# Kernel optimization log

Hardware: AMD Instinct MI355X
Metric: run time of the kernel (lower is better)

The kernel has to match this reference:

```python
import jax, jax.numpy as jnp
import numpy as np

LN_EPS = 1e-5


def layer_norm(x, gamma, beta):
    mu = jnp.mean(x, axis=-1, keepdims=True)
    var = jnp.mean(jnp.square(x - mu), axis=-1, keepdims=True)
    return (x - mu) * jax.lax.rsqrt(var + LN_EPS) * gamma + beta


def setup_inputs() -> dict:
    key = jax.random.key(0)
    ks = jax.random.split(key, 4)
    b, t, d, h, r = 4, 2048, 1024, 4096, 32
    x = jax.random.normal(ks[0], (b, t, d), dtype=jnp.float32)
    L = jax.random.normal(ks[1], (d, r), dtype=jnp.float32) * (1.0 / np.sqrt(d))
    W1 = jax.random.normal(ks[2], (d, h), dtype=jnp.float32) * (1.0 / np.sqrt(d))
    W2 = jax.random.normal(ks[3], (h, d), dtype=jnp.float32) * (1.0 / np.sqrt(h))
    return {
        "x": x, "L": L,
        "W1": W1, "b1": jnp.zeros((h,), jnp.float32),
        "W2": W2, "b2": jnp.zeros((d,), jnp.float32),
        "gamma1": jnp.ones((d,), jnp.float32), "beta1": jnp.zeros((d,), jnp.float32),
        "gamma2": jnp.ones((d,), jnp.float32), "beta2": jnp.zeros((d,), jnp.float32),
    }


def reference(x, L, W1, b1, W2, b2, gamma1, beta1, gamma2, beta2):
    d = x.shape[-1]
    # --- GeodesicAttention on norm1(x) ---
    hn = layer_norm(x, gamma1, beta1)  # (b,t,d)
    g = jnp.eye(d, dtype=x.dtype) + L @ L.T  # PSD metric G = I + L L^T, (d,d)
    # dist_sq[b,i,j] = (x_i - x_j)^T G (x_i - x_j)
    #               = q_i + q_j - 2 x_i^T G x_j   (quadratic expansion; avoids (b,t,t,d) diff tensor)
    xg = jnp.einsum('btd,de->bte', hn, g)          # G x, (b,t,d)
    q = jnp.einsum('btd,btd->bt', xg, hn)          # diag quadratic form, (b,t)
    cross = jnp.einsum('bid,bjd->bij', xg, hn)     # x_i^T G x_j, (b,t,t)
    dist_sq = q[:, :, None] + q[:, None, :] - 2.0 * cross
    attn = jax.nn.softmax(-dist_sq, axis=-1)       # (b,t,t)
    x = x + jnp.einsum('bij,bjd->bid', attn, hn)
    # --- MLP on norm2(x) ---
    hm = layer_norm(x, gamma2, beta2)
    hid = jax.nn.gelu(hm @ W1 + b1, approximate=False)
    x = x + hid @ W2 + b2
    return x
```

## Files before the change

kernel.cpp:

```cpp
#include <hip/hip_runtime.h>
#include <cstdint>

typedef float f32x4 __attribute__((ext_vector_type(4)));
typedef __bf16 bf16x8 __attribute__((ext_vector_type(8)));

#define AS1 __attribute__((address_space(1)))
#define AS3 __attribute__((address_space(3)))

__device__ __forceinline__ void gld_lds16(const void* g, void* l) {
    __builtin_amdgcn_global_load_lds((const AS1 void*)g, (AS3 void*)l, 16, 0, 0);
}

__device__ __forceinline__ unsigned short f2bf(float f) {
    unsigned u = __builtin_bit_cast(unsigned, f);
    u = u + 0x7fffu + ((u >> 16) & 1u);
    return (unsigned short)(u >> 16);
}
__device__ __forceinline__ float bf2f(unsigned short h) {
    unsigned u = ((unsigned)h) << 16;
    return __builtin_bit_cast(float, u);
}

__device__ __forceinline__ void bar() {
    asm volatile("" ::: "memory");
    __builtin_amdgcn_s_barrier();
    asm volatile("" ::: "memory");
}

#define WAITVM(n) asm volatile("s_waitcnt vmcnt(" #n ")" ::: "memory")
#define LGKM0     asm volatile("s_waitcnt lgkmcnt(0)" ::: "memory")
#define SCHED0    __builtin_amdgcn_sched_barrier(0)

template<int BN, int MODE>
__global__ __launch_bounds__(512, 2) void gemm8p(
    const unsigned short* __restrict__ A, long lda, long sAb,
    const unsigned short* __restrict__ B, long ldb, long sBb,
    void* C, long ldc, long sCb,
    const float* add, long ldadd, long sAddb,
    const float* __restrict__ bias, int K)
{
    constexpr int NR   = BN / 64;
    constexpr int ABUF = 256 * 128;
    constexpr int BBUF = BN * 128;
    constexpr int BUF  = ABUF + BBUF;
    __shared__ char sm[2 * BUF];
    const int tid = threadIdx.x, lane = tid & 63, wid = tid >> 6;
    const int wr = wid >> 2, wc = wid & 3;

    const long zb = blockIdx.z;
    const int nwg  = gridDim.x * gridDim.y;
    const int orig = blockIdx.y * gridDim.x + blockIdx.x;
    const int q8 = nwg >> 3, r8 = nwg & 7;
    const int xcd = orig & 7;
    const int wg  = (xcd < r8 ? xcd * (q8 + 1) : r8 * (q8 + 1) + (xcd - r8) * q8) + (orig >> 3);
    const int bx = wg % gridDim.x, by = wg / gridDim.x;

    const char* Ab = (const char*)(A + zb * sAb + (long)by * 256 * lda);
    const char* Bb = (const char*)(B + zb * sBb + (long)bx * BN * ldb);
    const long ldaB = lda * 2, ldbB = ldb * 2;

    auto stageA = [&](int kt, int p, int half) {
#pragma unroll
        for (int i = 0; i < 2; ++i) {
            const int r0 = half * 64 + i * 128;
            const int r  = r0 + (tid >> 3);
            gld_lds16(Ab + (long)r * ldaB + (long)kt * 128 + (((tid & 7) ^ (r & 7)) << 4),
                      sm + p * BUF + r0 * 128 + wid * 1024);
        }
    };
    auto stageB = [&](int kt, int p, int ks) {
#pragma unroll
        for (int i = 0; i < BN / 128; ++i) {
            const int r = i * 128 + (tid >> 2);
            gld_lds16(Bb + (long)r * ldbB + (long)kt * 128 + ks * 64 + (((tid & 3) ^ ((r >> 1) & 3)) << 4),
                      sm + p * BUF + ABUF + ks * BN * 64 + i * 8192 + wid * 1024);
        }
    };

    f32x4 acc[8][NR] = {};
    const int NT = K / 64;

#define PHASE(MH, KS, STAGE_STMT) do {                                          \
    bf16x8 af[4]; bf16x8 bfr[NR];                                               \
    _Pragma("unroll")                                                           \
    for (int m = 0; m < 4; ++m) {                                               \
        const int R = wr * 128 + ((MH) * 4 + m) * 16 + (lane & 15);             \
        const int cc = (((KS) * 4 + (lane >> 4)) ^ (R & 7)) << 4;               \
        af[m] = *(const bf16x8*)(bufp + R * 128 + cc);                          \
    }                                                                           \
    _Pragma("unroll")                                                           \
    for (int n = 0; n < NR; ++n) {                                              \
        const int R = wc * 16 * NR + n * 16 + (lane & 15);                      \
        const int cc = ((lane >> 4) ^ ((R >> 1) & 3)) << 4;                     \
        bfr[n] = *(const bf16x8*)(bufp + ABUF + (KS) * BN * 64 + R * 64 + cc);  \
    }                                                                           \
    STAGE_STMT;                                                                 \
    if (t < NT - 2) { if constexpr (BN == 256) WAITVM(8); else WAITVM(6); }     \
    else WAITVM(0);                                                             \
    bar();                                                                      \
    LGKM0; SCHED0;                                                              \
    __builtin_amdgcn_s_setprio(1);                                              \
    _Pragma("unroll")                                                           \
    for (int m = 0; m < 4; ++m)                                                 \
    _Pragma("unroll")                                                           \
        for (int n = 0; n < NR; ++n)                                            \
            acc[(MH) * 4 + m][n] = __builtin_amdgcn_mfma_f32_16x16x32_bf16(     \
                af[m], bfr[n], acc[(MH) * 4 + m][n], 0, 0, 0);                  \
    __builtin_amdgcn_s_setprio(0);                                              \
    bar();                                                                      \
} while (0)

    stageA(0, 0, 0); stageA(0, 0, 1); stageB(0, 0, 0); stageB(0, 0, 1);
    stageA(1, 1, 0); stageB(1, 1, 0); stageA(1, 1, 1); stageB(1, 1, 1);
    if constexpr (BN == 256) WAITVM(8); else WAITVM(6);
    bar();

#pragma unroll 1
    for (int t = 0; t < NT; ++t) {
        const int p = t & 1;
        const char* bufp = sm + p * BUF;
        PHASE(0, 0, { if (t >= 1 && t + 1 < NT) stageA(t + 1, p ^ 1, 1); });
        PHASE(1, 0, { if (t >= 1 && t + 1 < NT) stageB(t + 1, p ^ 1, 1); });
        PHASE(0, 1, { if (t + 2 < NT) stageB(t + 2, p, 0); });
        PHASE(1, 1, { if (t + 2 < NT) stageA(t + 2, p, 0); });
    }
#undef PHASE

    const long row0 = (long)by * 256 + wr * 128 + (lane >> 4) * 4;
    const long col0 = (long)bx * BN + wc * 16 * NR + (lane & 15);
#pragma unroll
    for (int m = 0; m < 8; ++m)
#pragma unroll
        for (int n = 0; n < NR; ++n)
#pragma unroll
            for (int j = 0; j < 4; ++j) {
                const long r = row0 + m * 16 + j;
                const long c = col0 + n * 16;
                const float v = acc[m][n][j];
                if (MODE == 0) {
                    ((float*)C)[zb * sCb + r * ldc + c] = v;
                } else if (MODE == 1) {
                    ((float*)C)[zb * sCb + r * ldc + c] = v + add[zb * sAddb + r * ldadd + c];
                } else if (MODE == 2) {
                    float tt = v + bias[c];
                    float gl = 0.5f * tt * (1.0f + erff(tt * 0.70710678118654752f));
                    ((unsigned short*)C)[zb * sCb + r * ldc + c] = f2bf(gl);
                } else {
                    ((float*)C)[zb * sCb + r * ldc + c] = v + bias[c] + add[zb * sAddb + r * ldadd + c];
                }
            }
}

__global__ __launch_bounds__(256) void ln_kernel(
    const float* __restrict__ x, const float* __restrict__ gamma, const float* __restrict__ beta,
    unsigned short* __restrict__ out, int ldout, float* qout, int pad)
{
    const int tid = threadIdx.x;
    const long row = blockIdx.x;
    float4 v = ((const float4*)(x + row * 1024))[tid];
    float s = v.x + v.y + v.z + v.w;
    float s2 = v.x * v.x + v.y * v.y + v.z * v.z + v.w * v.w;
#pragma unroll
    for (int off = 32; off; off >>= 1) {
        s  += __shfl_down(s, off);
        s2 += __shfl_down(s2, off);
    }
    __shared__ float red[12];
    const int lane = tid & 63, wid = tid >> 6;
    if (lane == 0) { red[wid] = s; red[4 + wid] = s2; }
    __syncthreads();
    s  = red[0] + red[1] + red[2] + red[3];
    s2 = red[4] + red[5] + red[6] + red[7];
    const float mu = s * (1.0f / 1024.0f);
    const float var = s2 * (1.0f / 1024.0f) - mu * mu;
    const float rs = rsqrtf(var + 1e-5f);
    const float4 g = ((const float4*)gamma)[tid];
    const float4 b = ((const float4*)beta)[tid];
    unsigned short o0 = f2bf((v.x - mu) * rs * g.x + b.x);
    unsigned short o1 = f2bf((v.y - mu) * rs * g.y + b.y);
    unsigned short o2 = f2bf((v.z - mu) * rs * g.z + b.z);
    unsigned short o3 = f2bf((v.w - mu) * rs * g.w + b.w);
    ushort4 ov; ov.x = o0; ov.y = o1; ov.z = o2; ov.w = o3;
    ((ushort4*)(out + row * (long)ldout))[tid] = ov;
    if (pad && tid < 32) out[row * (long)ldout + 1056 + tid] = 0;
    if (qout) {
        float y0 = bf2f(o0), y1 = bf2f(o1), y2 = bf2f(o2), y3 = bf2f(o3);
        float sq = y0 * y0 + y1 * y1 + y2 * y2 + y3 * y3;
#pragma unroll
        for (int off = 32; off; off >>= 1) sq += __shfl_down(sq, off);
        if (lane == 0) red[8 + wid] = sq;
        __syncthreads();
        if (tid == 0) qout[row] = red[8] + red[9] + red[10] + red[11];
    }
}

__global__ __launch_bounds__(256) void u_kernel(
    unsigned short* __restrict__ z, const float* __restrict__ L, float* __restrict__ q)
{
    const int tid = threadIdx.x;
    const long row = blockIdx.x;
    __shared__ float hn[1024];
    __shared__ float part[8][32];
    ushort4 uv = ((const ushort4*)(z + row * 1088))[tid];
    hn[tid * 4 + 0] = bf2f(uv.x);
    hn[tid * 4 + 1] = bf2f(uv.y);
    hn[tid * 4 + 2] = bf2f(uv.z);
    hn[tid * 4 + 3] = bf2f(uv.w);
    __syncthreads();
    const int j = tid & 31, grp = tid >> 5;
    float acc = 0.f;
    const float* Lp = L + j;
#pragma unroll 4
    for (int d = grp * 128; d < grp * 128 + 128; ++d)
        acc += hn[d] * Lp[(long)d * 32];
    part[grp][j] = acc;
    __syncthreads();
    if (tid < 32) {
        float u = 0.f;
#pragma unroll
        for (int g2 = 0; g2 < 8; ++g2) u += part[g2][tid];
        unsigned short ub = f2bf(u);
        z[row * 1088 + 1024 + tid] = ub;
        float uf = bf2f(ub);
        part[0][tid] = uf * uf;
    }
    __syncthreads();
    if (tid == 0) {
        float sq = 0.f;
#pragma unroll
        for (int t2 = 0; t2 < 32; ++t2) sq += part[0][t2];
        q[row] += sq;
    }
}

__global__ __launch_bounds__(256) void softmax_kernel(
    float* S, const float* qb)
{
    const int tid = threadIdx.x;
    const long i = blockIdx.x, bl = blockIdx.y;
    float* Sr = S + (bl * 2048 + i) * 2048;
    const float* qr = qb + bl * 2048;
    float l[8];
    float mx = -1e30f;
#pragma unroll
    for (int c2 = 0; c2 < 8; ++c2) {
        const int jj = tid + c2 * 256;
        l[c2] = 2.0f * Sr[jj] - qr[jj];
        mx = fmaxf(mx, l[c2]);
    }
#pragma unroll
    for (int off = 32; off; off >>= 1) mx = fmaxf(mx, __shfl_xor(mx, off));
    __shared__ float red[8];
    const int lane = tid & 63, wid = tid >> 6;
    if (lane == 0) red[wid] = mx;
    __syncthreads();
    mx = fmaxf(fmaxf(red[0], red[1]), fmaxf(red[2], red[3]));
    float sum = 0.f;
#pragma unroll
    for (int c2 = 0; c2 < 8; ++c2) { l[c2] = __expf(l[c2] - mx); sum += l[c2]; }
#pragma unroll
    for (int off = 32; off; off >>= 1) sum += __shfl_xor(sum, off);
    if (lane == 0) red[4 + wid] = sum;
    __syncthreads();
    sum = red[4] + red[5] + red[6] + red[7];
    const float inv = 1.0f / sum;
    unsigned short* Pr = (unsigned short*)S + (bl * 2048 + i) * 4096;
#pragma unroll
    for (int c2 = 0; c2 < 8; ++c2)
        Pr[tid + c2 * 256] = f2bf(l[c2] * inv);
}

__global__ __launch_bounds__(256) void transpose_v_kernel(
    const unsigned short* __restrict__ z, unsigned short* __restrict__ Vt, long sVtb)
{
    __shared__ unsigned short t[32][33];
    const int tid = threadIdx.x;
    const int tx = tid & 31, ty = tid >> 5;
    const long b = blockIdx.z;
    const long k0 = (long)blockIdx.x * 32, n0 = (long)blockIdx.y * 32;
#pragma unroll
    for (int r = 0; r < 32; r += 8)
        t[r + ty][tx] = z[(b * 2048 + k0 + r + ty) * 1088 + n0 + tx];
    __syncthreads();
#pragma unroll
    for (int r = 0; r < 32; r += 8)
        Vt[b * sVtb + (n0 + r + ty) * 2048 + k0 + tx] = t[tx][r + ty];
}

__global__ __launch_bounds__(256) void cast_transpose_kernel(
    const float* __restrict__ W, unsigned short* __restrict__ Wt, int rows, int cols)
{
    __shared__ float t[32][33];
    const int tid = threadIdx.x;
    const int tx = tid & 31, ty = tid >> 5;
    const long r0 = (long)blockIdx.y * 32, c0 = (long)blockIdx.x * 32;
#pragma unroll
    for (int r = 0; r < 32; r += 8)
        t[r + ty][tx] = W[(r0 + r + ty) * (long)cols + c0 + tx];
    __syncthreads();
#pragma unroll
    for (int r = 0; r < 32; r += 8)
        Wt[(c0 + r + ty) * (long)rows + r0 + tx] = f2bf(t[tx][r + ty]);
}

extern "C" void kernel_launch(void* const* d_in, const int* in_sizes, int n_in,
                              void* d_out, int out_size, void* d_ws, size_t ws_size,
                              hipStream_t stream)
{
    const float* x   = (const float*)d_in[0];
    const float* L   = (const float*)d_in[1];
    const float* W1  = (const float*)d_in[2];
    const float* b1  = (const float*)d_in[3];
    const float* W2  = (const float*)d_in[4];
    const float* b2  = (const float*)d_in[5];
    const float* g1  = (const float*)d_in[6];
    const float* be1 = (const float*)d_in[7];
    const float* g2  = (const float*)d_in[8];
    const float* be2 = (const float*)d_in[9];
    float* out = (float*)d_out;
    unsigned short* z = (unsigned short*)d_out;

    char* wsp = (char*)d_ws;
    float* q = (float*)wsp;
    char* pool = wsp + 32768;
    unsigned short* Vt   = (unsigned short*)pool;
    float*          Smat = (float*)(pool + 16777216);
    unsigned short* W1t = (unsigned short*)pool;
    unsigned short* W2t = (unsigned short*)(pool + 8388608);
    unsigned short* hm  = (unsigned short*)(pool + 16777216);
    unsigned short* hid = (unsigned short*)(pool + 33554432);
    const bool fullMLP = ws_size >= (size_t)32768 + 100663296 + 65536;

    ln_kernel<<<8192, 256, 0, stream>>>(x, g1, be1, z, 1088, q, 1);
    u_kernel<<<8192, 256, 0, stream>>>(z, L, q);

    transpose_v_kernel<<<dim3(64, 32, 4), 256, 0, stream>>>(z, Vt, (long)1024 * 2048);
    gemm8p<256, 0><<<dim3(8, 8, 4), 512, 0, stream>>>(
        z, 1088, (long)2048 * 1088,
        z, 1088, (long)2048 * 1088,
        Smat, 2048, (long)2048 * 2048,
        nullptr, 0, 0, nullptr, 1088);
    softmax_kernel<<<dim3(2048, 4), 256, 0, stream>>>(Smat, q);
    gemm8p<128, 1><<<dim3(8, 8, 4), 512, 0, stream>>>(
        (const unsigned short*)Smat, 4096, (long)2048 * 4096,
        Vt, 2048, (long)1024 * 2048,
        out, 1024, (long)2048 * 1024,
        x, 1024, (long)2048 * 1024,
        nullptr, 2048);

    cast_transpose_kernel<<<dim3(128, 32), 256, 0, stream>>>(W1, W1t, 1024, 4096);
    cast_transpose_kernel<<<dim3(32, 128), 256, 0, stream>>>(W2, W2t, 4096, 1024);
    ln_kernel<<<8192, 256, 0, stream>>>(out, g2, be2, hm, 1024, nullptr, 0);
    if (fullMLP) {
        gemm8p<256, 2><<<dim3(16, 32, 1), 512, 0, stream>>>(
            hm, 1024, 0, W1t, 1024, 0,
            hid, 4096, 0, nullptr, 0, 0, b1, 1024);
        gemm8p<128, 3><<<dim3(8, 32, 1), 512, 0, stream>>>(
            hid, 4096, 0, W2t, 4096, 0,
            out, 1024, 0, out, 1024, 0, b2, 4096);
    } else {
        for (int c = 0; c < 2; ++c) {
            const unsigned short* hmc = hm + (size_t)c * 4096 * 1024;
            float* oc = out + (size_t)c * 4096 * 1024;
            gemm8p<256, 2><<<dim3(16, 16, 1), 512, 0, stream>>>(
                hmc, 1024, 0, W1t, 1024, 0,
                hid, 4096, 0, nullptr, 0, 0, b1, 1024);
            gemm8p<128, 3><<<dim3(8, 16, 1), 512, 0, stream>>>(
                hid, 4096, 0, W2t, 4096, 0,
                oc, 1024, 0, oc, 1024, 0, b2, 4096);
        }
    }
}
```

Before: 389.5 us.

## Restructure GEMM prefetch waits and add XCD-aware tile swizzle for attention GEMMs

Changes the GEMM software pipeline so the prologue only preloads half of tile 1 and the loop issues the remaining stages every iteration. The vmcnt wait moves from every phase to one wait per K-tile at the last phase, which cuts per-phase stalls. Separately, a new swizzle mode maps the batched 8x8x4 attention GEMM grid so that each XCD gets a 2x4 block of neighbouring tiles within one batch, improving L2 reuse. The risk is that the wait counts are tightly coupled to the load ordering, and a miscount would cause stale LDS reads.

```diff
diff --git a/kernel.cpp b/kernel.cpp
--- a/kernel.cpp
+++ b/kernel.cpp
@@ -31,8 +31,8 @@
 #define LGKM0     asm volatile("s_waitcnt lgkmcnt(0)" ::: "memory")
 #define SCHED0    __builtin_amdgcn_sched_barrier(0)
 
-template<int BN, int MODE>
-__global__ __launch_bounds__(512, 2) void gemm8p(
+template<int BN, int MODE, int SWZ>
+__global__ __launch_bounds__(512, 2) void gemm8q(
     const unsigned short* __restrict__ A, long lda, long sAb,
     const unsigned short* __restrict__ B, long ldb, long sBb,
     void* C, long ldc, long sCb,
@@ -47,13 +47,24 @@
     const int tid = threadIdx.x, lane = tid & 63, wid = tid >> 6;
     const int wr = wid >> 2, wc = wid & 3;
 
-    const long zb = blockIdx.z;
-    const int nwg  = gridDim.x * gridDim.y;
-    const int orig = blockIdx.y * gridDim.x + blockIdx.x;
-    const int q8 = nwg >> 3, r8 = nwg & 7;
-    const int xcd = orig & 7;
-    const int wg  = (xcd < r8 ? xcd * (q8 + 1) : r8 * (q8 + 1) + (xcd - r8) * q8) + (orig >> 3);
-    const int bx = wg % gridDim.x, by = wg / gridDim.x;
+    int bx, by;
+    long zb;
+    if constexpr (SWZ == 1) {
+        const int d   = blockIdx.x + ((blockIdx.y + (blockIdx.z << 3)) << 3);
+        const int xcd = d & 7, j = d >> 3;
+        zb = j >> 3;
+        const int pos = j & 7;
+        by = ((xcd & 1) << 2) + (pos >> 1);
+        bx = ((xcd >> 1) << 1) + (pos & 1);
+    } else {
+        zb = blockIdx.z;
+        const int nwg  = gridDim.x * gridDim.y;
+        const int orig = blockIdx.y * gridDim.x + blockIdx.x;
+        const int q8 = nwg >> 3, r8 = nwg & 7;
+        const int xcd = orig & 7;
+        const int wg  = (xcd < r8 ? xcd * (q8 + 1) : r8 * (q8 + 1) + (xcd - r8) * q8) + (orig >> 3);
+        bx = wg % gridDim.x; by = wg / gridDim.x;
+    }
 
     const char* Ab = (const char*)(A + zb * sAb + (long)by * 256 * lda);
     const char* Bb = (const char*)(B + zb * sBb + (long)bx * BN * ldb);
@@ -80,7 +91,7 @@
     f32x4 acc[8][NR] = {};
     const int NT = K / 64;
 
-#define PHASE(MH, KS, STAGE_STMT) do {                                          \
+#define PHASE(MH, KS, STAGE_STMT, WAIT_STMT) do {                               \
     bf16x8 af[4]; bf16x8 bfr[NR];                                               \
     _Pragma("unroll")                                                           \
     for (int m = 0; m < 4; ++m) {                                               \
@@ -95,8 +106,7 @@
         bfr[n] = *(const bf16x8*)(bufp + ABUF + (KS) * BN * 64 + R * 64 + cc);  \
     }                                                                           \
     STAGE_STMT;                                                                 \
-    if (t < NT - 2) { if constexpr (BN == 256) WAITVM(8); else WAITVM(6); }     \
-    else WAITVM(0);                                                             \
+    WAIT_STMT;                                                                  \
     bar();                                                                      \
     LGKM0; SCHED0;                                                              \
     __builtin_amdgcn_s_setprio(1);                                              \
@@ -111,18 +121,20 @@
 } while (0)
 
     stageA(0, 0, 0); stageA(0, 0, 1); stageB(0, 0, 0); stageB(0, 0, 1);
-    stageA(1, 1, 0); stageB(1, 1, 0); stageA(1, 1, 1); stageB(1, 1, 1);
-    if constexpr (BN == 256) WAITVM(8); else WAITVM(6);
+    if (NT > 1) { stageB(1, 1, 0); stageA(1, 1, 0); }
+    if constexpr (BN == 256) WAITVM(4); else WAITVM(3);
     bar();
 
 #pragma unroll 1
     for (int t = 0; t < NT; ++t) {
         const int p = t & 1;
         const char* bufp = sm + p * BUF;
-        PHASE(0, 0, { if (t >= 1 && t + 1 < NT) stageA(t + 1, p ^ 1, 1); });
-        PHASE(1, 0, { if (t >= 1 && t + 1 < NT) stageB(t + 1, p ^ 1, 1); });
-        PHASE(0, 1, { if (t + 2 < NT) stageB(t + 2, p, 0); });
-        PHASE(1, 1, { if (t + 2 < NT) stageA(t + 2, p, 0); });
+        PHASE(0, 0, { if (t + 1 < NT) stageA(t + 1, p ^ 1, 1); }, {});
+        PHASE(1, 0, { if (t + 1 < NT) stageB(t + 1, p ^ 1, 1); }, {});
+        PHASE(0, 1, { if (t + 2 < NT) stageB(t + 2, p, 0); }, {});
+        PHASE(1, 1, { if (t + 2 < NT) stageA(t + 2, p, 0); },
+              { if (t + 2 < NT) { if constexpr (BN == 256) WAITVM(4); else WAITVM(3); }
+                else if (t + 1 < NT) WAITVM(0); });
     }
 #undef PHASE
 
@@ -335,13 +347,13 @@
     u_kernel<<<8192, 256, 0, stream>>>(z, L, q);
 
     transpose_v_kernel<<<dim3(64, 32, 4), 256, 0, stream>>>(z, Vt, (long)1024 * 2048);
-    gemm8p<256, 0><<<dim3(8, 8, 4), 512, 0, stream>>>(
+    gemm8q<256, 0, 1><<<dim3(8, 8, 4), 512, 0, stream>>>(
         z, 1088, (long)2048 * 1088,
         z, 1088, (long)2048 * 1088,
         Smat, 2048, (long)2048 * 2048,
         nullptr, 0, 0, nullptr, 1088);
     softmax_kernel<<<dim3(2048, 4), 256, 0, stream>>>(Smat, q);
-    gemm8p<128, 1><<<dim3(8, 8, 4), 512, 0, stream>>>(
+    gemm8q<128, 1, 1><<<dim3(8, 8, 4), 512, 0, stream>>>(
         (const unsigned short*)Smat, 4096, (long)2048 * 4096,
         Vt, 2048, (long)1024 * 2048,
         out, 1024, (long)2048 * 1024,
@@ -352,20 +364,20 @@
     cast_transpose_kernel<<<dim3(32, 128), 256, 0, stream>>>(W2, W2t, 4096, 1024);
     ln_kernel<<<8192, 256, 0, stream>>>(out, g2, be2, hm, 1024, nullptr, 0);
     if (fullMLP) {
-        gemm8p<256, 2><<<dim3(16, 32, 1), 512, 0, stream>>>(
+        gemm8q<256, 2, 0><<<dim3(16, 32, 1), 512, 0, stream>>>(
             hm, 1024, 0, W1t, 1024, 0,
             hid, 4096, 0, nullptr, 0, 0, b1, 1024);
-        gemm8p<128, 3><<<dim3(8, 32, 1), 512, 0, stream>>>(
+        gemm8q<128, 3, 0><<<dim3(8, 32, 1), 512, 0, stream>>>(
             hid, 4096, 0, W2t, 4096, 0,
             out, 1024, 0, out, 1024, 0, b2, 4096);
     } else {
         for (int c = 0; c < 2; ++c) {
             const unsigned short* hmc = hm + (size_t)c * 4096 * 1024;
             float* oc = out + (size_t)c * 4096 * 1024;
-            gemm8p<256, 2><<<dim3(16, 16, 1), 512, 0, stream>>>(
+            gemm8q<256, 2, 0><<<dim3(16, 16, 1), 512, 0, stream>>>(
                 hmc, 1024, 0, W1t, 1024, 0,
                 hid, 4096, 0, nullptr, 0, 0, b1, 1024);
-            gemm8p<128, 3><<<dim3(8, 16, 1), 512, 0, stream>>>(
+            gemm8q<128, 3, 0><<<dim3(8, 16, 1), 512, 0, stream>>>(
                 hid, 4096, 0, W2t, 4096, 0,
                 oc, 1024, 0, oc, 1024, 0, b2, 4096);
         }
```

Result: faster. 375.4 us (-3.6%).

## Switch GEMMs to triple-buffered LDS pipeline with fixed 256x128 tiles

Applied to the files above, without the earlier changes.

Replaces the double-buffered GEMM with a three-stage LDS ring buffer. Loads run two k-tiles ahead, and the kernel waits on vmcnt only once per k-tile instead of in every phase. The N tile is fixed at 128 for every GEMM, so the score GEMM and the MLP up-projection now launch twice as many workgroups. LDS use rises to 3*48KB per block, which may limit occupancy to fewer than two blocks per CU, and the smaller tile reduces operand reuse for the larger GEMMs.

```diff
diff --git a/kernel.cpp b/kernel.cpp
--- a/kernel.cpp
+++ b/kernel.cpp
@@ -31,19 +31,19 @@
 #define LGKM0     asm volatile("s_waitcnt lgkmcnt(0)" ::: "memory")
 #define SCHED0    __builtin_amdgcn_sched_barrier(0)
 
-template<int BN, int MODE>
-__global__ __launch_bounds__(512, 2) void gemm8p(
+template<int MODE>
+__global__ __launch_bounds__(512, 2) void gemm3r(
     const unsigned short* __restrict__ A, long lda, long sAb,
     const unsigned short* __restrict__ B, long ldb, long sBb,
     void* C, long ldc, long sCb,
     const float* add, long ldadd, long sAddb,
     const float* __restrict__ bias, int K)
 {
-    constexpr int NR   = BN / 64;
+    constexpr int NR   = 2;
     constexpr int ABUF = 256 * 128;
-    constexpr int BBUF = BN * 128;
+    constexpr int BBUF = 128 * 128;
     constexpr int BUF  = ABUF + BBUF;
-    __shared__ char sm[2 * BUF];
+    __shared__ char sm[3 * BUF];
     const int tid = threadIdx.x, lane = tid & 63, wid = tid >> 6;
     const int wr = wid >> 2, wc = wid & 3;
 
@@ -56,31 +56,28 @@
     const int bx = wg % gridDim.x, by = wg / gridDim.x;
 
     const char* Ab = (const char*)(A + zb * sAb + (long)by * 256 * lda);
-    const char* Bb = (const char*)(B + zb * sBb + (long)bx * BN * ldb);
+    const char* Bb = (const char*)(B + zb * sBb + (long)bx * 128 * ldb);
     const long ldaB = lda * 2, ldbB = ldb * 2;
 
-    auto stageA = [&](int kt, int p, int half) {
+    auto stageA = [&](int kt, int b, int half) {
 #pragma unroll
         for (int i = 0; i < 2; ++i) {
             const int r0 = half * 64 + i * 128;
             const int r  = r0 + (tid >> 3);
             gld_lds16(Ab + (long)r * ldaB + (long)kt * 128 + (((tid & 7) ^ (r & 7)) << 4),
-                      sm + p * BUF + r0 * 128 + wid * 1024);
+                      sm + b * BUF + r0 * 128 + wid * 1024);
         }
     };
-    auto stageB = [&](int kt, int p, int ks) {
-#pragma unroll
-        for (int i = 0; i < BN / 128; ++i) {
-            const int r = i * 128 + (tid >> 2);
-            gld_lds16(Bb + (long)r * ldbB + (long)kt * 128 + ks * 64 + (((tid & 3) ^ ((r >> 1) & 3)) << 4),
-                      sm + p * BUF + ABUF + ks * BN * 64 + i * 8192 + wid * 1024);
-        }
+    auto stageB = [&](int kt, int b, int ks) {
+        const int r = tid >> 2;
+        gld_lds16(Bb + (long)r * ldbB + (long)kt * 128 + ks * 64 + (((tid & 3) ^ ((r >> 1) & 3)) << 4),
+                  sm + b * BUF + ABUF + ks * 8192 + wid * 1024);
     };
 
     f32x4 acc[8][NR] = {};
     const int NT = K / 64;
 
-#define PHASE(MH, KS, STAGE_STMT) do {                                          \
+#define PHASE(MH, KS, STAGE_STMT, WAIT_STMT) do {                               \
     bf16x8 af[4]; bf16x8 bfr[NR];                                               \
     _Pragma("unroll")                                                           \
     for (int m = 0; m < 4; ++m) {                                               \
@@ -92,11 +89,10 @@
     for (int n = 0; n < NR; ++n) {                                              \
         const int R = wc * 16 * NR + n * 16 + (lane & 15);                      \
         const int cc = ((lane >> 4) ^ ((R >> 1) & 3)) << 4;                     \
-        bfr[n] = *(const bf16x8*)(bufp + ABUF + (KS) * BN * 64 + R * 64 + cc);  \
+        bfr[n] = *(const bf16x8*)(bufp + ABUF + (KS) * 8192 + R * 64 + cc);     \
     }                                                                           \
     STAGE_STMT;                                                                 \
-    if (t < NT - 2) { if constexpr (BN == 256) WAITVM(8); else WAITVM(6); }     \
-    else WAITVM(0);                                                             \
+    WAIT_STMT;                                                                  \
     bar();                                                                      \
     LGKM0; SCHED0;                                                              \
     __builtin_amdgcn_s_setprio(1);                                              \
@@ -111,23 +107,25 @@
 } while (0)
 
     stageA(0, 0, 0); stageA(0, 0, 1); stageB(0, 0, 0); stageB(0, 0, 1);
-    stageA(1, 1, 0); stageB(1, 1, 0); stageA(1, 1, 1); stageB(1, 1, 1);
-    if constexpr (BN == 256) WAITVM(8); else WAITVM(6);
+    stageA(1, 1, 0); stageA(1, 1, 1); stageB(1, 1, 0); stageB(1, 1, 1);
+    WAITVM(6);
     bar();
 
 #pragma unroll 1
     for (int t = 0; t < NT; ++t) {
-        const int p = t & 1;
-        const char* bufp = sm + p * BUF;
-        PHASE(0, 0, { if (t >= 1 && t + 1 < NT) stageA(t + 1, p ^ 1, 1); });
-        PHASE(1, 0, { if (t >= 1 && t + 1 < NT) stageB(t + 1, p ^ 1, 1); });
-        PHASE(0, 1, { if (t + 2 < NT) stageB(t + 2, p, 0); });
-        PHASE(1, 1, { if (t + 2 < NT) stageA(t + 2, p, 0); });
+        const int bi = t % 3, bs = (t + 2) % 3;
+        const char* bufp = sm + bi * BUF;
+        const bool st = (t + 2 < NT);
+        PHASE(0, 0, { if (st) stageA(t + 2, bs, 0); }, {});
+        PHASE(1, 0, { if (st) stageA(t + 2, bs, 1); }, {});
+        PHASE(0, 1, { if (st) stageB(t + 2, bs, 0); }, {});
+        PHASE(1, 1, { if (st) stageB(t + 2, bs, 1); },
+              { if (st) WAITVM(6); else if (t + 1 < NT) WAITVM(0); });
     }
 #undef PHASE
 
     const long row0 = (long)by * 256 + wr * 128 + (lane >> 4) * 4;
-    const long col0 = (long)bx * BN + wc * 16 * NR + (lane & 15);
+    const long col0 = (long)bx * 128 + wc * 16 * NR + (lane & 15);
 #pragma unroll
     for (int m = 0; m < 8; ++m)
 #pragma unroll
@@ -335,13 +333,13 @@
     u_kernel<<<8192, 256, 0, stream>>>(z, L, q);
 
     transpose_v_kernel<<<dim3(64, 32, 4), 256, 0, stream>>>(z, Vt, (long)1024 * 2048);
-    gemm8p<256, 0><<<dim3(8, 8, 4), 512, 0, stream>>>(
+    gemm3r<0><<<dim3(16, 8, 4), 512, 0, stream>>>(
         z, 1088, (long)2048 * 1088,
         z, 1088, (long)2048 * 1088,
         Smat, 2048, (long)2048 * 2048,
         nullptr, 0, 0, nullptr, 1088);
     softmax_kernel<<<dim3(2048, 4), 256, 0, stream>>>(Smat, q);
-    gemm8p<128, 1><<<dim3(8, 8, 4), 512, 0, stream>>>(
+    gemm3r<1><<<dim3(8, 8, 4), 512, 0, stream>>>(
         (const unsigned short*)Smat, 4096, (long)2048 * 4096,
         Vt, 2048, (long)1024 * 2048,
         out, 1024, (long)2048 * 1024,
@@ -352,20 +350,20 @@
     cast_transpose_kernel<<<dim3(32, 128), 256, 0, stream>>>(W2, W2t, 4096, 1024);
     ln_kernel<<<8192, 256, 0, stream>>>(out, g2, be2, hm, 1024, nullptr, 0);
     if (fullMLP) {
-        gemm8p<256, 2><<<dim3(16, 32, 1), 512, 0, stream>>>(
+        gemm3r<2><<<dim3(32, 32, 1), 512, 0, stream>>>(
             hm, 1024, 0, W1t, 1024, 0,
             hid, 4096, 0, nullptr, 0, 0, b1, 1024);
-        gemm8p<128, 3><<<dim3(8, 32, 1), 512, 0, stream>>>(
+        gemm3r<3><<<dim3(8, 32, 1), 512, 0, stream>>>(
             hid, 4096, 0, W2t, 4096, 0,
             out, 1024, 0, out, 1024, 0, b2, 4096);
     } else {
         for (int c = 0; c < 2; ++c) {
             const unsigned short* hmc = hm + (size_t)c * 4096 * 1024;
             float* oc = out + (size_t)c * 4096 * 1024;
-            gemm8p<256, 2><<<dim3(16, 16, 1), 512, 0, stream>>>(
+            gemm3r<2><<<dim3(32, 16, 1), 512, 0, stream>>>(
                 hmc, 1024, 0, W1t, 1024, 0,
                 hid, 4096, 0, nullptr, 0, 0, b1, 1024);
-            gemm8p<128, 3><<<dim3(8, 16, 1), 512, 0, stream>>>(
+            gemm3r<3><<<dim3(8, 16, 1), 512, 0, stream>>>(
                 hid, 4096, 0, W2t, 4096, 0,
                 oc, 1024, 0, oc, 1024, 0, b2, 4096);
         }
```

Measured after the change: 397.6 us. +2.1%, slower.
